# Performance work log

Measured on AMD Instinct MI355X. Metric: run time of the kernel, lower is better.

Reference implementation:

```python
import jax, jax.numpy as jnp
import numpy as np

N = 2048
E = 32768
IN_CH = 512
HID = 64
HEADS = 4
OUT_CH = 64
NUM_HOPS = 2
BETA = 0.5
NEG_SLOPE = 0.2
LN_EPS = 1e-5


def setup_inputs() -> dict:
    key = jax.random.key(0)
    ks = jax.random.split(key, 12)
    x = jax.random.normal(ks[0], (N, IN_CH), jnp.float32)
    edge_index = jax.random.randint(ks[1], (2, E), 0, N, dtype=jnp.int32)
    g = lambda k, shape, fan_in: jax.random.normal(k, shape, jnp.float32) * (1.0 / np.sqrt(fan_in))
    return {
        'x': x,
        'edge_index': edge_index,
        'l1_lin_w': g(ks[2], (NUM_HOPS, IN_CH, HEADS * HID), IN_CH),
        'l1_att_src': g(ks[3], (NUM_HOPS, HEADS, HID), HID),
        'l1_att_dst': g(ks[4], (NUM_HOPS, HEADS, HID), HID),
        'l1_hop_att': jnp.ones((NUM_HOPS,), jnp.float32),
        'l1_bias': g(ks[5], (HEADS * HID,), HEADS * HID),
        'l2_lin_w': g(ks[6], (NUM_HOPS, HEADS * HID, OUT_CH), HEADS * HID),
        'l2_att_src': g(ks[7], (NUM_HOPS, 1, OUT_CH), OUT_CH),
        'l2_att_dst': g(ks[8], (NUM_HOPS, 1, OUT_CH), OUT_CH),
        'l2_hop_att': jnp.ones((NUM_HOPS,), jnp.float32),
        'l2_res_w': g(ks[9], (HEADS * HID, OUT_CH), HEADS * HID),
        'l2_ln_scale': jnp.ones((OUT_CH,), jnp.float32),
        'l2_ln_bias': jnp.zeros((OUT_CH,), jnp.float32),
        'l2_bias': g(ks[10], (OUT_CH,), OUT_CH),
    }


def _leaky(v):
    return jnp.where(v >= 0, v, NEG_SLOPE * v)


def _masked_softmax_src(score, mask):
    # PyG softmax(alpha, edge_index[1]): normalize over src (axis 0) per dst column.
    s = jnp.where(mask[:, :, None], score, -jnp.inf)
    s = s - jnp.max(s, axis=0, keepdims=True)  # diag always valid -> finite max
    e = jnp.exp(s)
    return e / jnp.sum(e, axis=0, keepdims=True)


def _mgat_conv(x, A, motif, lin_w, att_src, att_dst, hop_att, heads, out_ch, concat,
               res_w=None, ln_scale=None, ln_bias=None, bias=None, residual=False):
    n = x.shape[0]
    hop_w = jax.nn.softmax(hop_att)
    eye = jnp.eye(n, dtype=bool)
    out = 0.0
    A_pow = A  # adj^(hop+1)
    for hop in range(NUM_HOPS):
        mask = (A_pow > 0) | eye  # remove_self_loops + add_self_loops -> diag always in
        hop_x = (x @ lin_w[hop]).reshape(n, heads, out_ch)
        s_src = jnp.einsum('nhc,hc->nh', hop_x, att_src[hop])
        s_dst = jnp.einsum('nhc,hc->nh', hop_x, att_dst[hop])
        score = s_src[:, None, :] + s_dst[None, :, :]  # [src, dst, h]
        a_first = _masked_softmax_src(_leaky(score), mask)
        a_motif = _masked_softmax_src(_leaky(score * motif[:, :, None]), mask)
        alpha = BETA * a_first + (1.0 - BETA) * a_motif
        hop_out = jnp.einsum('sdh,shc->dhc', alpha, hop_x)  # scatter-add at dst
        out = out + hop_w[hop] * hop_out
        A_pow = A_pow @ A
    if concat:
        out = out.reshape(n, heads * out_ch)
    else:
        out = out.mean(axis=1)
    if residual:
        res = x @ res_w if res_w is not None else x
        out = out + res
        mu = jnp.mean(out, axis=-1, keepdims=True)
        var = jnp.mean((out - mu) ** 2, axis=-1, keepdims=True)
        out = (out - mu) / jnp.sqrt(var + LN_EPS) * ln_scale + ln_bias
    if bias is not None:
        out = out + bias
    return out


def reference(x, edge_index, l1_lin_w, l1_att_src, l1_att_dst, l1_hop_att, l1_bias,
              l2_lin_w, l2_att_src, l2_att_dst, l2_hop_att, l2_res_w,
              l2_ln_scale, l2_ln_bias, l2_bias):
    n = x.shape[0]
    A = jnp.zeros((n, n), x.dtype).at[edge_index[0], edge_index[1]].set(1.0)
    motif = A @ A @ A
    motif = motif / jnp.maximum(motif.sum(axis=-1, keepdims=True), 1.0)
    h = _mgat_conv(x, A, motif, l1_lin_w, l1_att_src, l1_att_dst, l1_hop_att,
                   heads=HEADS, out_ch=HID, concat=True, bias=l1_bias, residual=False)
    h = jax.nn.elu(h)  # dropout p in eval mode -> identity
    out = _mgat_conv(h, A, motif, l2_lin_w, l2_att_src, l2_att_dst, l2_hop_att,
                     heads=1, out_ch=OUT_CH, concat=False,
                     res_w=l2_res_w, ln_scale=l2_ln_scale, ln_bias=l2_ln_bias,
                     bias=l2_bias, residual=True)
    return out
```

## Files before the change

kernel.cpp:

```cpp
#include <hip/hip_runtime.h>

namespace {

constexpr int kN = 2048;
constexpr int kWords = kN / 64;
constexpr int kC1 = 256;
constexpr int kC2 = 64;
constexpr int kIN = 512;
constexpr float kNegSlope = 0.2f;
constexpr float kLnEps = 1e-5f;

__device__ __forceinline__ float leakyf(float v) {
  return v >= 0.f ? v : kNegSlope * v;
}
__device__ __forceinline__ void onl(float& m, float& l, float v) {
  if (v > m) { l = l * __expf(m - v) + 1.f; m = v; }
  else       { l += __expf(v - m); }
}
__device__ __forceinline__ void mergeml(float& M, float& L, float m, float l) {
  if (m > M) { L = L * __expf(M - m) + l; M = m; }
  else       { L += l * __expf(m - M); }
}
__device__ __forceinline__ float bf2f(unsigned short u) {
  union { unsigned int i; float f; } v; v.i = ((unsigned int)u) << 16; return v.f;
}
__device__ __forceinline__ unsigned short f2bf(float f) {
  unsigned int u = __float_as_uint(f);
  unsigned int r = u + 0x7fffu + ((u >> 16) & 1u);
  return (unsigned short)(r >> 16);
}

__global__ void build_bits(const int* __restrict__ ei, int E,
                           unsigned long long* rowbits, unsigned long long* colbitsT) {
  int e = blockIdx.x * 256 + threadIdx.x;
  if (e >= E) return;
  int s = ei[e], d = ei[E + e];
  atomicOr(&rowbits[(size_t)s * kWords + (d >> 6)], 1ull << (d & 63));
  atomicOr(&colbitsT[(size_t)(s >> 6) * kN + d], 1ull << (s & 63));
}

__global__ __launch_bounds__(256) void a2_tiled(
    const unsigned long long* __restrict__ rowbits,
    const unsigned long long* __restrict__ colbitsT,
    unsigned short* __restrict__ A2,
    unsigned long long* __restrict__ colbits2T) {
  int bx = blockIdx.x, by = blockIdx.y;
  int t = threadIdx.x;
  __shared__ unsigned long long rb[64][33];
  __shared__ unsigned long long cb[32][64];
  __shared__ unsigned long long cw[64];
  int s0 = by * 64, d0 = bx * 64;
  for (int i = t; i < 64 * 32; i += 256) {
    int ss = i >> 5, w = i & 31;
    rb[ss][w] = rowbits[(size_t)(s0 + ss) * kWords + w];
  }
  for (int i = t; i < 32 * 64; i += 256) {
    int w = i >> 6, dd = i & 63;
    cb[w][dd] = colbitsT[(size_t)w * kN + d0 + dd];
  }
  if (t < 64) cw[t] = 0ull;
  __syncthreads();
  int tx = t & 15, ty4 = (t >> 4) * 4;
  int acc[4][4] = {};
#pragma unroll 4
  for (int w = 0; w < 32; ++w) {
    unsigned long long r0 = rb[ty4 + 0][w], r1 = rb[ty4 + 1][w];
    unsigned long long r2 = rb[ty4 + 2][w], r3 = rb[ty4 + 3][w];
    unsigned long long c0 = cb[w][tx], c1 = cb[w][tx + 16];
    unsigned long long c2 = cb[w][tx + 32], c3 = cb[w][tx + 48];
    acc[0][0] += __popcll(r0 & c0); acc[0][1] += __popcll(r0 & c1);
    acc[0][2] += __popcll(r0 & c2); acc[0][3] += __popcll(r0 & c3);
    acc[1][0] += __popcll(r1 & c0); acc[1][1] += __popcll(r1 & c1);
    acc[1][2] += __popcll(r1 & c2); acc[1][3] += __popcll(r1 & c3);
    acc[2][0] += __popcll(r2 & c0); acc[2][1] += __popcll(r2 & c1);
    acc[2][2] += __popcll(r2 & c2); acc[2][3] += __popcll(r2 & c3);
    acc[3][0] += __popcll(r3 & c0); acc[3][1] += __popcll(r3 & c1);
    acc[3][2] += __popcll(r3 & c2); acc[3][3] += __popcll(r3 & c3);
  }
#pragma unroll
  for (int i = 0; i < 4; ++i)
#pragma unroll
    for (int j = 0; j < 4; ++j)
      A2[(size_t)(s0 + ty4 + i) * kN + d0 + tx + 16 * j] = (unsigned short)acc[i][j];
#pragma unroll
  for (int j = 0; j < 4; ++j) {
    unsigned long long m = 0;
#pragma unroll
    for (int i = 0; i < 4; ++i)
      if (acc[i][j]) m |= 1ull << (ty4 + i);
    if (m) atomicOr(&cw[tx + 16 * j], m);
  }
  __syncthreads();
  if (t < 64) colbits2T[(size_t)by * kN + d0 + t] = cw[t];
}

__global__ __launch_bounds__(256) void a3_dense(
    const unsigned long long* __restrict__ rowbits,
    const unsigned short* __restrict__ A2,
    unsigned short* __restrict__ a3u,
    float* __restrict__ invr) {
  int s = blockIdx.x;
  int t = threadIdx.x;
  int lane = t & 63;
  __shared__ unsigned short jl[kN];
  __shared__ int jtot_s;
  __shared__ float redv[4];
  if (t < 64) {
    unsigned long long word = (lane < kWords) ? rowbits[(size_t)s * kWords + lane] : 0ull;
    int c = __popcll(word);
    int inc = c;
    for (int o = 1; o < 64; o <<= 1) { int v = __shfl_up(inc, o); if (lane >= o) inc += v; }
    if (lane == 63) jtot_s = inc;
    int off = inc - c;
    int base = lane * 64;
    while (word) {
      int b = __builtin_ctzll(word);
      word &= word - 1;
      jl[off++] = (unsigned short)(base + b);
    }
  }
  __syncthreads();
  int jtot = jtot_s;
  const uint4* a2v = reinterpret_cast<const uint4*>(A2);
  uint4 acc = make_uint4(0u, 0u, 0u, 0u);
  int ji = 0;
  for (; ji + 4 <= jtot; ji += 4) {
    uint4 v0 = a2v[(size_t)jl[ji + 0] * 256 + t];
    uint4 v1 = a2v[(size_t)jl[ji + 1] * 256 + t];
    uint4 v2 = a2v[(size_t)jl[ji + 2] * 256 + t];
    uint4 v3 = a2v[(size_t)jl[ji + 3] * 256 + t];
    acc.x += v0.x + v1.x + v2.x + v3.x;
    acc.y += v0.y + v1.y + v2.y + v3.y;
    acc.z += v0.z + v1.z + v2.z + v3.z;
    acc.w += v0.w + v1.w + v2.w + v3.w;
  }
  for (; ji < jtot; ++ji) {
    uint4 v = a2v[(size_t)jl[ji] * 256 + t];
    acc.x += v.x; acc.y += v.y; acc.z += v.z; acc.w += v.w;
  }
  reinterpret_cast<uint4*>(a3u)[(size_t)s * 256 + t] = acc;
  float tot = (float)((acc.x & 0xffffu) + (acc.x >> 16) +
                      (acc.y & 0xffffu) + (acc.y >> 16) +
                      (acc.z & 0xffffu) + (acc.z >> 16) +
                      (acc.w & 0xffffu) + (acc.w >> 16));
  for (int o = 32; o; o >>= 1) tot += __shfl_xor(tot, o);
  if (lane == 0) redv[t >> 6] = tot;
  __syncthreads();
  if (t == 0)
    invr[s] = 1.f / fmaxf(redv[0] + redv[1] + redv[2] + redv[3], 1.f);
}

__global__ __launch_bounds__(256) void transpose_motif(
    const unsigned short* __restrict__ a3u, const float* __restrict__ invr,
    float* __restrict__ motifT) {
  __shared__ float tile[64][65];
  __shared__ float invs[64];
  int d0 = blockIdx.x * 64, s0 = blockIdx.y * 64;
  int t = threadIdx.x;
  int tx = t & 63, ty = t >> 6;
  if (t < 64) invs[t] = invr[s0 + t];
  __syncthreads();
#pragma unroll
  for (int i = 0; i < 64; i += 4)
    tile[ty + i][tx] = (float)a3u[(size_t)(s0 + ty + i) * kN + d0 + tx] * invs[ty + i];
  __syncthreads();
#pragma unroll
  for (int i = 0; i < 64; i += 4)
    motifT[(size_t)(d0 + ty + i) * kN + s0 + tx] = tile[tx][ty + i];
}

__global__ __launch_bounds__(256) void gemm1(
    const float* __restrict__ x, const float* __restrict__ l1w,
    unsigned short* __restrict__ hx1b,
    const float* __restrict__ l1as, const float* __restrict__ l1ad,
    float* __restrict__ ss1, float* __restrict__ sd1) {
  int hop = blockIdx.z;
  int row0 = blockIdx.y * 32, col0 = blockIdx.x * 64;
  const float* B = l1w + (size_t)hop * kIN * kC1;
  unsigned short* Cz = hx1b + (size_t)hop * kN * kC1;
  __shared__ float As[2][32][20];
  __shared__ float Bs[2][16][68];
  int t = threadIdx.x;
  int tx = t & 15, ty = t >> 4;
  int am = t >> 2, ak = (t & 3) * 4;
  int bk = t >> 4, bn = (t & 15) * 4;
  float4 ra, rb;
  if (t < 128)
    ra = *reinterpret_cast<const float4*>(x + (size_t)(row0 + am) * kIN + ak);
  rb = *reinterpret_cast<const float4*>(B + (size_t)bk * kC1 + col0 + bn);
  if (t < 128)
    *reinterpret_cast<float4*>(&As[0][am][ak]) = ra;
  *reinterpret_cast<float4*>(&Bs[0][bk][bn]) = rb;
  __syncthreads();
  float acc[2][4] = {};
  int cur = 0;
  for (int k0 = 16; k0 <= kIN; k0 += 16) {
    bool more = (k0 < kIN);
    if (more) {
      if (t < 128)
        ra = *reinterpret_cast<const float4*>(x + (size_t)(row0 + am) * kIN + k0 + ak);
      rb = *reinterpret_cast<const float4*>(B + (size_t)(k0 + bk) * kC1 + col0 + bn);
    }
#pragma unroll
    for (int kk = 0; kk < 16; ++kk) {
      float a0 = As[cur][ty * 2 + 0][kk];
      float a1 = As[cur][ty * 2 + 1][kk];
      float4 b = *reinterpret_cast<const float4*>(&Bs[cur][kk][tx * 4]);
      acc[0][0] += a0 * b.x; acc[0][1] += a0 * b.y;
      acc[0][2] += a0 * b.z; acc[0][3] += a0 * b.w;
      acc[1][0] += a1 * b.x; acc[1][1] += a1 * b.y;
      acc[1][2] += a1 * b.z; acc[1][3] += a1 * b.w;
    }
    if (more) {
      if (t < 128)
        *reinterpret_cast<float4*>(&As[cur ^ 1][am][ak]) = ra;
      *reinterpret_cast<float4*>(&Bs[cur ^ 1][bk][bn]) = rb;
      __syncthreads();
      cur ^= 1;
    }
  }
#pragma unroll
  for (int i = 0; i < 2; ++i) {
    ushort4 pb;
    pb.x = f2bf(acc[i][0]); pb.y = f2bf(acc[i][1]);
    pb.z = f2bf(acc[i][2]); pb.w = f2bf(acc[i][3]);
    *reinterpret_cast<ushort4*>(Cz + (size_t)(row0 + ty * 2 + i) * kC1 + col0 + tx * 4) = pb;
  }
  int h = col0 >> 6;
  float as_[4], ad_[4];
#pragma unroll
  for (int j = 0; j < 4; ++j) {
    as_[j] = l1as[hop * kC1 + col0 + tx * 4 + j];
    ad_[j] = l1ad[hop * kC1 + col0 + tx * 4 + j];
  }
#pragma unroll
  for (int i = 0; i < 2; ++i) {
    float ps = acc[i][0] * as_[0] + acc[i][1] * as_[1] +
               acc[i][2] * as_[2] + acc[i][3] * as_[3];
    float pd = acc[i][0] * ad_[0] + acc[i][1] * ad_[1] +
               acc[i][2] * ad_[2] + acc[i][3] * ad_[3];
#pragma unroll
    for (int o = 1; o < 16; o <<= 1) {
      ps += __shfl_xor(ps, o);
      pd += __shfl_xor(pd, o);
    }
    if (tx == 0) {
      int n = row0 + ty * 2 + i;
      ss1[((size_t)hop * kN + n) * 4 + h] = ps;
      sd1[((size_t)hop * kN + n) * 4 + h] = pd;
    }
  }
}

__global__ __launch_bounds__(256) void gemm2(
    const float* __restrict__ A, const float* __restrict__ l2w,
    const float* __restrict__ l2rw, unsigned short* __restrict__ hx2b,
    float* __restrict__ resOut,
    const float* __restrict__ attS, const float* __restrict__ attD,
    float* __restrict__ ssO, float* __restrict__ sdO) {
  int z = blockIdx.z;
  const float* B = (z < 2) ? l2w + (size_t)z * kC1 * kC2 : l2rw;
  __shared__ float As[2][16][20];
  __shared__ float Bs[2][16][68];
  int t = threadIdx.x;
  int tx = t & 15, ty = t >> 4;
  int row0 = blockIdx.y * 16;
  int am = t >> 2, ak = (t & 3) * 4;
  int bk = t >> 4, bn = (t & 15) * 4;
  float4 ra, rb;
  if (t < 64)
    ra = *reinterpret_cast<const float4*>(A + (size_t)(row0 + am) * kC1 + ak);
  rb = *reinterpret_cast<const float4*>(B + (size_t)bk * kC2 + bn);
  if (t < 64)
    *reinterpret_cast<float4*>(&As[0][am][ak]) = ra;
  *reinterpret_cast<float4*>(&Bs[0][bk][bn]) = rb;
  __syncthreads();
  float acc[4] = {};
  int cur = 0;
  for (int k0 = 16; k0 <= kC1; k0 += 16) {
    bool more = (k0 < kC1);
    if (more) {
      if (t < 64)
        ra = *reinterpret_cast<const float4*>(A + (size_t)(row0 + am) * kC1 + k0 + ak);
      rb = *reinterpret_cast<const float4*>(B + (size_t)(k0 + bk) * kC2 + bn);
    }
#pragma unroll
    for (int kk = 0; kk < 16; ++kk) {
      float a = As[cur][ty][kk];
      float4 b = *reinterpret_cast<const float4*>(&Bs[cur][kk][tx * 4]);
      acc[0] += a * b.x; acc[1] += a * b.y;
      acc[2] += a * b.z; acc[3] += a * b.w;
    }
    if (more) {
      if (t < 64)
        *reinterpret_cast<float4*>(&As[cur ^ 1][am][ak]) = ra;
      *reinterpret_cast<float4*>(&Bs[cur ^ 1][bk][bn]) = rb;
      __syncthreads();
      cur ^= 1;
    }
  }
  if (z < 2) {
    ushort4 pb;
    pb.x = f2bf(acc[0]); pb.y = f2bf(acc[1]);
    pb.z = f2bf(acc[2]); pb.w = f2bf(acc[3]);
    *reinterpret_cast<ushort4*>(hx2b + (size_t)z * kN * kC2 +
                                (size_t)(row0 + ty) * kC2 + tx * 4) = pb;
    float as_[4], ad_[4];
#pragma unroll
    for (int j = 0; j < 4; ++j) {
      as_[j] = attS[z * kC2 + tx * 4 + j];
      ad_[j] = attD[z * kC2 + tx * 4 + j];
    }
    float ps = acc[0] * as_[0] + acc[1] * as_[1] + acc[2] * as_[2] + acc[3] * as_[3];
    float pd = acc[0] * ad_[0] + acc[1] * ad_[1] + acc[2] * ad_[2] + acc[3] * ad_[3];
#pragma unroll
    for (int o = 1; o < 16; o <<= 1) {
      ps += __shfl_xor(ps, o);
      pd += __shfl_xor(pd, o);
    }
    if (tx == 0) {
      int n = row0 + ty;
      ssO[(size_t)z * kN + n] = ps;
      sdO[(size_t)z * kN + n] = pd;
    }
  } else {
    float4 c = make_float4(acc[0], acc[1], acc[2], acc[3]);
    *reinterpret_cast<float4*>(resOut + (size_t)(row0 + ty) * kC2 + tx * 4) = c;
  }
}

__global__ __launch_bounds__(256) void agg_l1(
    const unsigned short* __restrict__ hxb,
    const float* __restrict__ ssrc,
    const float* __restrict__ sdst,
    const float* __restrict__ motifT,
    const unsigned long long* __restrict__ colbitsT,
    const unsigned long long* __restrict__ colbits2T,
    const float* __restrict__ hop_att,
    const float* __restrict__ bias,
    float* __restrict__ hbuf) {
  int d = blockIdx.x;
  int t = threadIdx.x;
  int lane = t & 63;
  int h = t >> 6;
  int cq = lane;
  int hq = cq >> 4;
  __shared__ unsigned short slist[kN];
  __shared__ float mrow[kN];
  __shared__ float w_lds[64 * 4];
  __shared__ int s_total;
  __shared__ float4 red4[4][64];
  {
    const float4* mp = reinterpret_cast<const float4*>(motifT + (size_t)d * kN);
    float4* mr = reinterpret_cast<float4*>(mrow);
    mr[t] = mp[t];
    mr[t + 256] = mp[t + 256];
  }
  float a0 = hop_att[0], a1 = hop_att[1];
  float mxa = fmaxf(a0, a1);
  float e0 = __expf(a0 - mxa), e1 = __expf(a1 - mxa);
  float wh0 = e0 / (e0 + e1), wh1 = e1 / (e0 + e1);
  float4 acc4 = make_float4(0.f, 0.f, 0.f, 0.f);
  for (int hop = 0; hop < 2; ++hop) {
    const unsigned long long* cm = hop ? colbits2T : colbitsT;
    if (t < 64) {
      unsigned long long word = (lane < kWords) ? cm[(size_t)lane * kN + d] : 0ull;
      if (lane == (d >> 6)) word |= 1ull << (d & 63);
      int cnt = __popcll(word);
      int inc = cnt;
      for (int o = 1; o < 64; o <<= 1) { int v = __shfl_up(inc, o); if (lane >= o) inc += v; }
      if (lane == 63) s_total = inc;
      int off = inc - cnt;
      int base = lane * 64;
      while (word) {
        int b = __builtin_ctzll(word);
        word &= word - 1;
        slist[off++] = (unsigned short)(base + b);
      }
    }
    __syncthreads();
    int total = s_total;
    float sd = sdst[((size_t)hop * kN + d) * 4 + h];
    const ushort4* hx4 = reinterpret_cast<const ushort4*>(hxb + (size_t)hop * kN * kC1);
    const float* ssp = ssrc + (size_t)hop * kN * 4;
    float m1 = -3.0e38f, l1v = 0.f, m2 = -3.0e38f, l2v = 0.f;
    for (int q = lane; q < total; q += 64) {
      int s = slist[q];
      float mv = mrow[s];
      float v = ssp[s * 4 + h] + sd;
      onl(m1, l1v, leakyf(v));
      onl(m2, l2v, leakyf(v * mv));
    }
#pragma unroll
    for (int o = 1; o < 64; o <<= 1) {
      float mm = __shfl_xor(m1, o), ll = __shfl_xor(l1v, o);
      mergeml(m1, l1v, mm, ll);
      float mm2 = __shfl_xor(m2, o), ll2 = __shfl_xor(l2v, o);
      mergeml(m2, l2v, mm2, ll2);
    }
    float il1 = 1.f / l1v, il2 = 1.f / l2v;
    float wh = hop ? wh1 : wh0;
    for (int c0 = 0; c0 < total; c0 += 64) {
      int nsi = min(64, total - c0);
      if (lane < nsi) {
        int s = slist[c0 + lane];
        float mv = mrow[s];
        float v = ssp[s * 4 + h] + sd;
        w_lds[lane * 4 + h] = (0.5f * __expf(leakyf(v) - m1) * il1 +
                               0.5f * __expf(leakyf(v * mv) - m2) * il2) * wh;
      }
      __syncthreads();
      int q = h;
      for (; q + 4 < nsi; q += 8) {
        int s0 = slist[c0 + q], s1 = slist[c0 + q + 4];
        ushort4 u0 = hx4[(size_t)s0 * 64 + cq];
        ushort4 u1 = hx4[(size_t)s1 * 64 + cq];
        float w0 = w_lds[q * 4 + hq], w1 = w_lds[(q + 4) * 4 + hq];
        acc4.x += w0 * bf2f(u0.x) + w1 * bf2f(u1.x);
        acc4.y += w0 * bf2f(u0.y) + w1 * bf2f(u1.y);
        acc4.z += w0 * bf2f(u0.z) + w1 * bf2f(u1.z);
        acc4.w += w0 * bf2f(u0.w) + w1 * bf2f(u1.w);
      }
      if (q < nsi) {
        int s0 = slist[c0 + q];
        ushort4 u0 = hx4[(size_t)s0 * 64 + cq];
        float w0 = w_lds[q * 4 + hq];
        acc4.x += w0 * bf2f(u0.x); acc4.y += w0 * bf2f(u0.y);
        acc4.z += w0 * bf2f(u0.z); acc4.w += w0 * bf2f(u0.w);
      }
      __syncthreads();
    }
    __syncthreads();
  }
  red4[h][cq] = acc4;
  __syncthreads();
  if (t < 64) {
    float4 a = red4[0][t], b = red4[1][t], c = red4[2][t], e = red4[3][t];
    float4 bv = reinterpret_cast<const float4*>(bias)[t];
    float4 v;
    v.x = a.x + b.x + c.x + e.x + bv.x;
    v.y = a.y + b.y + c.y + e.y + bv.y;
    v.z = a.z + b.z + c.z + e.z + bv.z;
    v.w = a.w + b.w + c.w + e.w + bv.w;
    v.x = v.x > 0.f ? v.x : __expf(v.x) - 1.f;
    v.y = v.y > 0.f ? v.y : __expf(v.y) - 1.f;
    v.z = v.z > 0.f ? v.z : __expf(v.z) - 1.f;
    v.w = v.w > 0.f ? v.w : __expf(v.w) - 1.f;
    reinterpret_cast<float4*>(hbuf)[(size_t)d * 64 + t] = v;
  }
}

__global__ __launch_bounds__(256) void agg_l2(
    const unsigned short* __restrict__ hxb,
    const float* __restrict__ ssrc,
    const float* __restrict__ sdst,
    const float* __restrict__ motifT,
    const unsigned long long* __restrict__ colbitsT,
    const unsigned long long* __restrict__ colbits2T,
    const float* __restrict__ hop_att,
    const float* __restrict__ res,
    const float* __restrict__ lns, const float* __restrict__ lnb,
    const float* __restrict__ l2b,
    float* __restrict__ out) {
  int d = blockIdx.x;
  int t = threadIdx.x;
  int lane = t & 63;
  int g = t >> 6;
  int cq = t & 15;
  int sg = t >> 4;
  __shared__ unsigned short slist[kN];
  __shared__ float mrow[kN];
  __shared__ float w_lds[64];
  __shared__ int s_total;
  __shared__ float4 red4[16][16];
  __shared__ float out_lds[64];
  __shared__ float smst[4][4];
  {
    const float4* mp = reinterpret_cast<const float4*>(motifT + (size_t)d * kN);
    float4* mr = reinterpret_cast<float4*>(mrow);
    mr[t] = mp[t];
    mr[t + 256] = mp[t + 256];
  }
  float a0 = hop_att[0], a1 = hop_att[1];
  float mxa = fmaxf(a0, a1);
  float e0 = __expf(a0 - mxa), e1 = __expf(a1 - mxa);
  float wh0 = e0 / (e0 + e1), wh1 = e1 / (e0 + e1);
  float4 acc4 = make_float4(0.f, 0.f, 0.f, 0.f);
  for (int hop = 0; hop < 2; ++hop) {
    const unsigned long long* cm = hop ? colbits2T : colbitsT;
    if (t < 64) {
      unsigned long long word = (lane < kWords) ? cm[(size_t)lane * kN + d] : 0ull;
      if (lane == (d >> 6)) word |= 1ull << (d & 63);
      int cnt = __popcll(word);
      int inc = cnt;
      for (int o = 1; o < 64; o <<= 1) { int v = __shfl_up(inc, o); if (lane >= o) inc += v; }
      if (lane == 63) s_total = inc;
      int off = inc - cnt;
      int base = lane * 64;
      while (word) {
        int b = __builtin_ctzll(word);
        word &= word - 1;
        slist[off++] = (unsigned short)(base + b);
      }
    }
    __syncthreads();
    int total = s_total;
    float sd = sdst[(size_t)hop * kN + d];
    const ushort4* hx4 = reinterpret_cast<const ushort4*>(hxb + (size_t)hop * kN * kC2);
    const float* ssp = ssrc + (size_t)hop * kN;
    float m1 = -3.0e38f, l1v = 0.f, m2 = -3.0e38f, l2v = 0.f;
    for (int q = t; q < total; q += 256) {
      int s = slist[q];
      float mv = mrow[s];
      float v = ssp[s] + sd;
      onl(m1, l1v, leakyf(v));
      onl(m2, l2v, leakyf(v * mv));
    }
#pragma unroll
    for (int o = 1; o < 64; o <<= 1) {
      float mm = __shfl_xor(m1, o), ll = __shfl_xor(l1v, o);
      mergeml(m1, l1v, mm, ll);
      float mm2 = __shfl_xor(m2, o), ll2 = __shfl_xor(l2v, o);
      mergeml(m2, l2v, mm2, ll2);
    }
    if (lane == 0) {
      smst[g][0] = m1; smst[g][1] = l1v; smst[g][2] = m2; smst[g][3] = l2v;
    }
    __syncthreads();
    float M1 = -3.0e38f, L1 = 0.f, M2 = -3.0e38f, L2 = 0.f;
#pragma unroll
    for (int gg = 0; gg < 4; ++gg) {
      mergeml(M1, L1, smst[gg][0], smst[gg][1]);
      mergeml(M2, L2, smst[gg][2], smst[gg][3]);
    }
    float il1 = 1.f / L1, il2 = 1.f / L2;
    float wh = hop ? wh1 : wh0;
    for (int c0 = 0; c0 < total; c0 += 64) {
      int nsi = min(64, total - c0);
      if (t < nsi) {
        int s = slist[c0 + t];
        float mv = mrow[s];
        float v = ssp[s] + sd;
        w_lds[t] = (0.5f * __expf(leakyf(v) - M1) * il1 +
                    0.5f * __expf(leakyf(v * mv) - M2) * il2) * wh;
      }
      __syncthreads();
      int q = sg;
      for (; q + 16 < nsi; q += 32) {
        int s0 = slist[c0 + q], s1 = slist[c0 + q + 16];
        ushort4 u0 = hx4[(size_t)s0 * 16 + cq];
        ushort4 u1 = hx4[(size_t)s1 * 16 + cq];
        float w0 = w_lds[q], w1 = w_lds[q + 16];
        acc4.x += w0 * bf2f(u0.x) + w1 * bf2f(u1.x);
        acc4.y += w0 * bf2f(u0.y) + w1 * bf2f(u1.y);
        acc4.z += w0 * bf2f(u0.z) + w1 * bf2f(u1.z);
        acc4.w += w0 * bf2f(u0.w) + w1 * bf2f(u1.w);
      }
      if (q < nsi) {
        int s0 = slist[c0 + q];
        ushort4 u0 = hx4[(size_t)s0 * 16 + cq];
        float w0 = w_lds[q];
        acc4.x += w0 * bf2f(u0.x); acc4.y += w0 * bf2f(u0.y);
        acc4.z += w0 * bf2f(u0.z); acc4.w += w0 * bf2f(u0.w);
      }
      __syncthreads();
    }
    __syncthreads();
  }
  red4[sg][cq] = acc4;
  __syncthreads();
  if (t < 16) {
    float4 v = make_float4(0.f, 0.f, 0.f, 0.f);
#pragma unroll
    for (int q = 0; q < 16; ++q) {
      float4 a = red4[q][t];
      v.x += a.x; v.y += a.y; v.z += a.z; v.w += a.w;
    }
    out_lds[t * 4 + 0] = v.x;
    out_lds[t * 4 + 1] = v.y;
    out_lds[t * 4 + 2] = v.z;
    out_lds[t * 4 + 3] = v.w;
  }
  __syncthreads();
  if (t < 64) {
    float v = out_lds[t] + res[(size_t)d * kC2 + t];
    float s = v;
    for (int o = 32; o; o >>= 1) s += __shfl_xor(s, o);
    float mu = s * (1.f / kC2);
    float dv = v - mu;
    float q = dv * dv;
    for (int o = 32; o; o >>= 1) q += __shfl_xor(q, o);
    float var = q * (1.f / kC2);
    out[(size_t)d * kC2 + t] = dv * rsqrtf(var + kLnEps) * lns[t] + lnb[t] + l2b[t];
  }
}

}

extern "C" void kernel_launch(void* const* d_in, const int* in_sizes, int n_in,
                              void* d_out, int out_size, void* d_ws, size_t ws_size,
                              hipStream_t stream) {
  const float* x    = (const float*)d_in[0];
  const int*   ei   = (const int*)d_in[1];
  const float* l1w  = (const float*)d_in[2];
  const float* l1as = (const float*)d_in[3];
  const float* l1ad = (const float*)d_in[4];
  const float* l1ha = (const float*)d_in[5];
  const float* l1b  = (const float*)d_in[6];
  const float* l2w  = (const float*)d_in[7];
  const float* l2as = (const float*)d_in[8];
  const float* l2ad = (const float*)d_in[9];
  const float* l2ha = (const float*)d_in[10];
  const float* l2rw = (const float*)d_in[11];
  const float* lns  = (const float*)d_in[12];
  const float* lnb  = (const float*)d_in[13];
  const float* l2b  = (const float*)d_in[14];
  int E = in_sizes[1] / 2;

  size_t o = 0;
  auto take = [&](size_t bytes) { size_t r = o; o += (bytes + 255) & ~(size_t)255; return r; };
  size_t oRB  = take((size_t)kN * kWords * 8);
  size_t oCB  = take((size_t)kWords * kN * 8);
  size_t zEnd = o;
  size_t oCB2 = take((size_t)kWords * kN * 8);
  size_t oA2  = take((size_t)kN * kN * 2);
  size_t oA3  = take((size_t)kN * kN * 2);
  size_t oINV = take((size_t)kN * 4);
  size_t oMFT = take((size_t)kN * kN * 4);
  size_t oHX1 = take((size_t)2 * kN * kC1 * 2);
  size_t oH   = take((size_t)kN * kC1 * 4);
  size_t oHX2 = take((size_t)2 * kN * kC2 * 2);
  size_t oRES = take((size_t)kN * kC2 * 4);
  size_t oSS1 = take((size_t)2 * kN * 4 * 4);
  size_t oSD1 = take((size_t)2 * kN * 4 * 4);
  size_t oSS2 = take((size_t)2 * kN * 4);
  size_t oSD2 = take((size_t)2 * kN * 4);
  if (ws_size < o) return;

  char* w = (char*)d_ws;
  unsigned long long* rowbits = (unsigned long long*)(w + oRB);
  unsigned long long* colbitsT = (unsigned long long*)(w + oCB);
  unsigned long long* colbits2T = (unsigned long long*)(w + oCB2);
  unsigned short* A2 = (unsigned short*)(w + oA2);
  unsigned short* A3u = (unsigned short*)(w + oA3);
  float* invr = (float*)(w + oINV);
  float* motifT = (float*)(w + oMFT);
  unsigned short* hx1b = (unsigned short*)(w + oHX1);
  float* hbuf = (float*)(w + oH);
  unsigned short* hx2b = (unsigned short*)(w + oHX2);
  float* res = (float*)(w + oRES);
  float* ss1 = (float*)(w + oSS1);
  float* sd1 = (float*)(w + oSD1);
  float* ss2 = (float*)(w + oSS2);
  float* sd2 = (float*)(w + oSD2);

  hipMemsetAsync(d_ws, 0, zEnd, stream);

  build_bits<<<(E + 255) / 256, 256, 0, stream>>>(ei, E, rowbits, colbitsT);
  a2_tiled<<<dim3(kN / 64, kN / 64), 256, 0, stream>>>(rowbits, colbitsT, A2, colbits2T);
  a3_dense<<<kN, 256, 0, stream>>>(rowbits, A2, A3u, invr);
  transpose_motif<<<dim3(kN / 64, kN / 64), 256, 0, stream>>>(A3u, invr, motifT);

  gemm1<<<dim3(kC1 / 64, kN / 32, 2), 256, 0, stream>>>(x, l1w, hx1b, l1as, l1ad, ss1, sd1);
  agg_l1<<<kN, 256, 0, stream>>>(hx1b, ss1, sd1, motifT, colbitsT, colbits2T,
                                 l1ha, l1b, hbuf);

  gemm2<<<dim3(1, kN / 16, 3), 256, 0, stream>>>(hbuf, l2w, l2rw, hx2b, res,
                                                 l2as, l2ad, ss2, sd2);
  agg_l2<<<kN, 256, 0, stream>>>(hx2b, ss2, sd2, motifT, colbitsT, colbits2T,
                                 l2ha, res, lns, lnb, l2b, (float*)d_out);
}
```

Before: 148.6 us.

## Double-buffer attention weights to drop a barrier per aggregation chunk

Both aggregation kernels now compute the softmax weights for the next 64-source chunk into a second LDS buffer while the current chunk is gathered, so each chunk needs one barrier instead of two. The first chunk's weights are computed in a prologue per hop. The extra end-of-hop barrier is removed and the l2 inner loop is restructured to match. This costs slightly more LDS and some register pressure from overlapping the weight computation with the gather.

```diff
diff --git a/kernel.cpp b/kernel.cpp
--- a/kernel.cpp
+++ b/kernel.cpp
@@ -347,7 +347,7 @@
   int hq = cq >> 4;
   __shared__ unsigned short slist[kN];
   __shared__ float mrow[kN];
-  __shared__ float w_lds[64 * 4];
+  __shared__ float w_lds[2][64 * 4];
   __shared__ int s_total;
   __shared__ float4 red4[4][64];
   {
@@ -400,22 +400,37 @@
     }
     float il1 = 1.f / l1v, il2 = 1.f / l2v;
     float wh = hop ? wh1 : wh0;
+    {
+      int nsi0 = min(64, total);
+      if (lane < nsi0) {
+        int s = slist[lane];
+        float mv = mrow[s];
+        float v = ssp[s * 4 + h] + sd;
+        w_lds[0][lane * 4 + h] = (0.5f * __expf(leakyf(v) - m1) * il1 +
+                                  0.5f * __expf(leakyf(v * mv) - m2) * il2) * wh;
+      }
+    }
+    __syncthreads();
+    int cur = 0;
     for (int c0 = 0; c0 < total; c0 += 64) {
       int nsi = min(64, total - c0);
-      if (lane < nsi) {
-        int s = slist[c0 + lane];
-        float mv = mrow[s];
-        float v = ssp[s * 4 + h] + sd;
-        w_lds[lane * 4 + h] = (0.5f * __expf(leakyf(v) - m1) * il1 +
-                               0.5f * __expf(leakyf(v * mv) - m2) * il2) * wh;
-      }
-      __syncthreads();
+      int c1 = c0 + 64;
+      if (c1 < total) {
+        int nsi1 = min(64, total - c1);
+        if (lane < nsi1) {
+          int s = slist[c1 + lane];
+          float mv = mrow[s];
+          float v = ssp[s * 4 + h] + sd;
+          w_lds[cur ^ 1][lane * 4 + h] = (0.5f * __expf(leakyf(v) - m1) * il1 +
+                                          0.5f * __expf(leakyf(v * mv) - m2) * il2) * wh;
+        }
+      }
       int q = h;
       for (; q + 4 < nsi; q += 8) {
         int s0 = slist[c0 + q], s1 = slist[c0 + q + 4];
         ushort4 u0 = hx4[(size_t)s0 * 64 + cq];
         ushort4 u1 = hx4[(size_t)s1 * 64 + cq];
-        float w0 = w_lds[q * 4 + hq], w1 = w_lds[(q + 4) * 4 + hq];
+        float w0 = w_lds[cur][q * 4 + hq], w1 = w_lds[cur][(q + 4) * 4 + hq];
         acc4.x += w0 * bf2f(u0.x) + w1 * bf2f(u1.x);
         acc4.y += w0 * bf2f(u0.y) + w1 * bf2f(u1.y);
         acc4.z += w0 * bf2f(u0.z) + w1 * bf2f(u1.z);
@@ -424,13 +439,13 @@
       if (q < nsi) {
         int s0 = slist[c0 + q];
         ushort4 u0 = hx4[(size_t)s0 * 64 + cq];
-        float w0 = w_lds[q * 4 + hq];
+        float w0 = w_lds[cur][q * 4 + hq];
         acc4.x += w0 * bf2f(u0.x); acc4.y += w0 * bf2f(u0.y);
         acc4.z += w0 * bf2f(u0.z); acc4.w += w0 * bf2f(u0.w);
       }
       __syncthreads();
-    }
-    __syncthreads();
+      cur ^= 1;
+    }
   }
   red4[h][cq] = acc4;
   __syncthreads();
@@ -470,7 +485,7 @@
   int sg = t >> 4;
   __shared__ unsigned short slist[kN];
   __shared__ float mrow[kN];
-  __shared__ float w_lds[64];
+  __shared__ float w_lds[2][64];
   __shared__ int s_total;
   __shared__ float4 red4[16][16];
   __shared__ float out_lds[64];
@@ -535,37 +550,53 @@
     }
     float il1 = 1.f / L1, il2 = 1.f / L2;
     float wh = hop ? wh1 : wh0;
+    {
+      int nsi0 = min(64, total);
+      if (t < nsi0) {
+        int s = slist[t];
+        float mv = mrow[s];
+        float v = ssp[s] + sd;
+        w_lds[0][t] = (0.5f * __expf(leakyf(v) - M1) * il1 +
+                       0.5f * __expf(leakyf(v * mv) - M2) * il2) * wh;
+      }
+    }
+    __syncthreads();
+    int cur = 0;
     for (int c0 = 0; c0 < total; c0 += 64) {
       int nsi = min(64, total - c0);
-      if (t < nsi) {
-        int s = slist[c0 + t];
-        float mv = mrow[s];
-        float v = ssp[s] + sd;
-        w_lds[t] = (0.5f * __expf(leakyf(v) - M1) * il1 +
-                    0.5f * __expf(leakyf(v * mv) - M2) * il2) * wh;
-      }
-      __syncthreads();
+      int c1 = c0 + 64;
+      if (c1 < total) {
+        int nsi1 = min(64, total - c1);
+        if (t < nsi1) {
+          int s = slist[c1 + t];
+          float mv = mrow[s];
+          float v = ssp[s] + sd;
+          w_lds[cur ^ 1][t] = (0.5f * __expf(leakyf(v) - M1) * il1 +
+                               0.5f * __expf(leakyf(v * mv) - M2) * il2) * wh;
+        }
+      }
       int q = sg;
-      for (; q + 16 < nsi; q += 32) {
+      if (q + 16 < nsi) {
         int s0 = slist[c0 + q], s1 = slist[c0 + q + 16];
         ushort4 u0 = hx4[(size_t)s0 * 16 + cq];
         ushort4 u1 = hx4[(size_t)s1 * 16 + cq];
-        float w0 = w_lds[q], w1 = w_lds[q + 16];
+        float w0 = w_lds[cur][q], w1 = w_lds[cur][q + 16];
         acc4.x += w0 * bf2f(u0.x) + w1 * bf2f(u1.x);
         acc4.y += w0 * bf2f(u0.y) + w1 * bf2f(u1.y);
         acc4.z += w0 * bf2f(u0.z) + w1 * bf2f(u1.z);
         acc4.w += w0 * bf2f(u0.w) + w1 * bf2f(u1.w);
-      }
-      if (q < nsi) {
+        q += 32;
+      }
+      for (; q < nsi; q += 16) {
         int s0 = slist[c0 + q];
         ushort4 u0 = hx4[(size_t)s0 * 16 + cq];
-        float w0 = w_lds[q];
+        float w0 = w_lds[cur][q];
         acc4.x += w0 * bf2f(u0.x); acc4.y += w0 * bf2f(u0.y);
         acc4.z += w0 * bf2f(u0.z); acc4.w += w0 * bf2f(u0.w);
       }
       __syncthreads();
-    }
-    __syncthreads();
+      cur ^= 1;
+    }
   }
   red4[sg][cq] = acc4;
   __syncthreads();
```

New measurement: 148.8 us. No clear change (+0.2%).

## Split aggregation kernels across two blocks per node with partial-sum combine

Applied to the files above, without the earlier changes.

Both attention aggregation kernels now launch two blocks per destination node. Each block handles half of the 64-source chunks and writes a partial sum. For layer 1, the bias+ELU epilogue moves into gemm2's A-load, which sums the two partials. For layer 2, a new combine kernel adds the partials and the residual, then applies LayerNorm. This doubles the grid to improve occupancy and load balance, at the cost of recomputing the softmax statistics and the motif-row load in both halves, extra partial-buffer traffic, and one more launch.

```diff
diff --git a/kernel.cpp b/kernel.cpp
--- a/kernel.cpp
+++ b/kernel.cpp
@@ -253,7 +253,9 @@
 }
 
 __global__ __launch_bounds__(256) void gemm2(
-    const float* __restrict__ A, const float* __restrict__ l2w,
+    const float* __restrict__ p1a, const float* __restrict__ p1b,
+    const float* __restrict__ l1b,
+    const float* __restrict__ l2w,
     const float* __restrict__ l2rw, unsigned short* __restrict__ hx2b,
     float* __restrict__ resOut,
     const float* __restrict__ attS, const float* __restrict__ attD,
@@ -267,9 +269,22 @@
   int row0 = blockIdx.y * 16;
   int am = t >> 2, ak = (t & 3) * 4;
   int bk = t >> 4, bn = (t & 15) * 4;
+  auto ldA = [&](int k) -> float4 {
+    size_t off = (size_t)(row0 + am) * kC1 + k + ak;
+    float4 a = *reinterpret_cast<const float4*>(p1a + off);
+    float4 b = *reinterpret_cast<const float4*>(p1b + off);
+    float4 c = *reinterpret_cast<const float4*>(l1b + k + ak);
+    float4 r;
+    r.x = a.x + b.x + c.x; r.y = a.y + b.y + c.y;
+    r.z = a.z + b.z + c.z; r.w = a.w + b.w + c.w;
+    r.x = r.x > 0.f ? r.x : __expf(r.x) - 1.f;
+    r.y = r.y > 0.f ? r.y : __expf(r.y) - 1.f;
+    r.z = r.z > 0.f ? r.z : __expf(r.z) - 1.f;
+    r.w = r.w > 0.f ? r.w : __expf(r.w) - 1.f;
+    return r;
+  };
   float4 ra, rb;
-  if (t < 64)
-    ra = *reinterpret_cast<const float4*>(A + (size_t)(row0 + am) * kC1 + ak);
+  if (t < 64) ra = ldA(0);
   rb = *reinterpret_cast<const float4*>(B + (size_t)bk * kC2 + bn);
   if (t < 64)
     *reinterpret_cast<float4*>(&As[0][am][ak]) = ra;
@@ -280,8 +295,7 @@
   for (int k0 = 16; k0 <= kC1; k0 += 16) {
     bool more = (k0 < kC1);
     if (more) {
-      if (t < 64)
-        ra = *reinterpret_cast<const float4*>(A + (size_t)(row0 + am) * kC1 + k0 + ak);
+      if (t < 64) ra = ldA(k0);
       rb = *reinterpret_cast<const float4*>(B + (size_t)(k0 + bk) * kC2 + bn);
     }
 #pragma unroll
@@ -337,9 +351,9 @@
     const unsigned long long* __restrict__ colbitsT,
     const unsigned long long* __restrict__ colbits2T,
     const float* __restrict__ hop_att,
-    const float* __restrict__ bias,
-    float* __restrict__ hbuf) {
+    float* __restrict__ part) {
   int d = blockIdx.x;
+  int half = blockIdx.y;
   int t = threadIdx.x;
   int lane = t & 63;
   int h = t >> 6;
@@ -400,7 +414,12 @@
     }
     float il1 = 1.f / l1v, il2 = 1.f / l2v;
     float wh = hop ? wh1 : wh0;
-    for (int c0 = 0; c0 < total; c0 += 64) {
+    int nch = (total + 63) >> 6;
+    int hc = (nch + 1) >> 1;
+    int cbeg = half * hc;
+    int cend = min(nch, cbeg + hc);
+    for (int ci = cbeg; ci < cend; ++ci) {
+      int c0 = ci * 64;
       int nsi = min(64, total - c0);
       if (lane < nsi) {
         int s = slist[c0 + lane];
@@ -436,17 +455,12 @@
   __syncthreads();
   if (t < 64) {
     float4 a = red4[0][t], b = red4[1][t], c = red4[2][t], e = red4[3][t];
-    float4 bv = reinterpret_cast<const float4*>(bias)[t];
     float4 v;
-    v.x = a.x + b.x + c.x + e.x + bv.x;
-    v.y = a.y + b.y + c.y + e.y + bv.y;
-    v.z = a.z + b.z + c.z + e.z + bv.z;
-    v.w = a.w + b.w + c.w + e.w + bv.w;
-    v.x = v.x > 0.f ? v.x : __expf(v.x) - 1.f;
-    v.y = v.y > 0.f ? v.y : __expf(v.y) - 1.f;
-    v.z = v.z > 0.f ? v.z : __expf(v.z) - 1.f;
-    v.w = v.w > 0.f ? v.w : __expf(v.w) - 1.f;
-    reinterpret_cast<float4*>(hbuf)[(size_t)d * 64 + t] = v;
+    v.x = a.x + b.x + c.x + e.x;
+    v.y = a.y + b.y + c.y + e.y;
+    v.z = a.z + b.z + c.z + e.z;
+    v.w = a.w + b.w + c.w + e.w;
+    reinterpret_cast<float4*>(part + ((size_t)half * kN + d) * kC1)[t] = v;
   }
 }
 
@@ -458,11 +472,9 @@
     const unsigned long long* __restrict__ colbitsT,
     const unsigned long long* __restrict__ colbits2T,
     const float* __restrict__ hop_att,
-    const float* __restrict__ res,
-    const float* __restrict__ lns, const float* __restrict__ lnb,
-    const float* __restrict__ l2b,
-    float* __restrict__ out) {
+    float* __restrict__ part) {
   int d = blockIdx.x;
+  int half = blockIdx.y;
   int t = threadIdx.x;
   int lane = t & 63;
   int g = t >> 6;
@@ -473,7 +485,6 @@
   __shared__ float w_lds[64];
   __shared__ int s_total;
   __shared__ float4 red4[16][16];
-  __shared__ float out_lds[64];
   __shared__ float smst[4][4];
   {
     const float4* mp = reinterpret_cast<const float4*>(motifT + (size_t)d * kN);
@@ -535,7 +546,12 @@
     }
     float il1 = 1.f / L1, il2 = 1.f / L2;
     float wh = hop ? wh1 : wh0;
-    for (int c0 = 0; c0 < total; c0 += 64) {
+    int nch = (total + 63) >> 6;
+    int hc = (nch + 1) >> 1;
+    int cbeg = half * hc;
+    int cend = min(nch, cbeg + hc);
+    for (int ci = cbeg; ci < cend; ++ci) {
+      int c0 = ci * 64;
       int nsi = min(64, total - c0);
       if (t < nsi) {
         int s = slist[c0 + t];
@@ -546,7 +562,7 @@
       }
       __syncthreads();
       int q = sg;
-      for (; q + 16 < nsi; q += 32) {
+      if (q + 16 < nsi) {
         int s0 = slist[c0 + q], s1 = slist[c0 + q + 16];
         ushort4 u0 = hx4[(size_t)s0 * 16 + cq];
         ushort4 u1 = hx4[(size_t)s1 * 16 + cq];
@@ -555,8 +571,9 @@
         acc4.y += w0 * bf2f(u0.y) + w1 * bf2f(u1.y);
         acc4.z += w0 * bf2f(u0.z) + w1 * bf2f(u1.z);
         acc4.w += w0 * bf2f(u0.w) + w1 * bf2f(u1.w);
-      }
-      if (q < nsi) {
+        q += 32;
+      }
+      for (; q < nsi; q += 16) {
         int s0 = slist[c0 + q];
         ushort4 u0 = hx4[(size_t)s0 * 16 + cq];
         float w0 = w_lds[q];
@@ -576,23 +593,28 @@
       float4 a = red4[q][t];
       v.x += a.x; v.y += a.y; v.z += a.z; v.w += a.w;
     }
-    out_lds[t * 4 + 0] = v.x;
-    out_lds[t * 4 + 1] = v.y;
-    out_lds[t * 4 + 2] = v.z;
-    out_lds[t * 4 + 3] = v.w;
-  }
-  __syncthreads();
-  if (t < 64) {
-    float v = out_lds[t] + res[(size_t)d * kC2 + t];
-    float s = v;
-    for (int o = 32; o; o >>= 1) s += __shfl_xor(s, o);
-    float mu = s * (1.f / kC2);
-    float dv = v - mu;
-    float q = dv * dv;
-    for (int o = 32; o; o >>= 1) q += __shfl_xor(q, o);
-    float var = q * (1.f / kC2);
-    out[(size_t)d * kC2 + t] = dv * rsqrtf(var + kLnEps) * lns[t] + lnb[t] + l2b[t];
-  }
+    reinterpret_cast<float4*>(part + ((size_t)half * kN + d) * kC2)[t] = v;
+  }
+}
+
+__global__ void combine_l2(
+    const float* __restrict__ part,
+    const float* __restrict__ res,
+    const float* __restrict__ lns, const float* __restrict__ lnb,
+    const float* __restrict__ l2b,
+    float* __restrict__ out) {
+  int d = blockIdx.x, t = threadIdx.x;
+  float v = part[((size_t)0 * kN + d) * kC2 + t] +
+            part[((size_t)1 * kN + d) * kC2 + t] +
+            res[(size_t)d * kC2 + t];
+  float s = v;
+  for (int o = 32; o; o >>= 1) s += __shfl_xor(s, o);
+  float mu = s * (1.f / kC2);
+  float dv = v - mu;
+  float q = dv * dv;
+  for (int o = 32; o; o >>= 1) q += __shfl_xor(q, o);
+  float var = q * (1.f / kC2);
+  out[(size_t)d * kC2 + t] = dv * rsqrtf(var + kLnEps) * lns[t] + lnb[t] + l2b[t];
 }
 
 }
@@ -628,8 +650,9 @@
   size_t oINV = take((size_t)kN * 4);
   size_t oMFT = take((size_t)kN * kN * 4);
   size_t oHX1 = take((size_t)2 * kN * kC1 * 2);
-  size_t oH   = take((size_t)kN * kC1 * 4);
+  size_t oP1  = take((size_t)2 * kN * kC1 * 4);
   size_t oHX2 = take((size_t)2 * kN * kC2 * 2);
+  size_t oP2  = take((size_t)2 * kN * kC2 * 4);
   size_t oRES = take((size_t)kN * kC2 * 4);
   size_t oSS1 = take((size_t)2 * kN * 4 * 4);
   size_t oSD1 = take((size_t)2 * kN * 4 * 4);
@@ -646,8 +669,9 @@
   float* invr = (float*)(w + oINV);
   float* motifT = (float*)(w + oMFT);
   unsigned short* hx1b = (unsigned short*)(w + oHX1);
-  float* hbuf = (float*)(w + oH);
+  float* p1 = (float*)(w + oP1);
   unsigned short* hx2b = (unsigned short*)(w + oHX2);
+  float* p2 = (float*)(w + oP2);
   float* res = (float*)(w + oRES);
   float* ss1 = (float*)(w + oSS1);
   float* sd1 = (float*)(w + oSD1);
@@ -662,11 +686,13 @@
   transpose_motif<<<dim3(kN / 64, kN / 64), 256, 0, stream>>>(A3u, invr, motifT);
 
   gemm1<<<dim3(kC1 / 64, kN / 32, 2), 256, 0, stream>>>(x, l1w, hx1b, l1as, l1ad, ss1, sd1);
-  agg_l1<<<kN, 256, 0, stream>>>(hx1b, ss1, sd1, motifT, colbitsT, colbits2T,
-                                 l1ha, l1b, hbuf);
-
-  gemm2<<<dim3(1, kN / 16, 3), 256, 0, stream>>>(hbuf, l2w, l2rw, hx2b, res,
+  agg_l1<<<dim3(kN, 2), 256, 0, stream>>>(hx1b, ss1, sd1, motifT, colbitsT, colbits2T,
+                                          l1ha, p1);
+
+  gemm2<<<dim3(1, kN / 16, 3), 256, 0, stream>>>(p1, p1 + (size_t)kN * kC1, l1b,
+                                                 l2w, l2rw, hx2b, res,
                                                  l2as, l2ad, ss2, sd2);
-  agg_l2<<<kN, 256, 0, stream>>>(hx2b, ss2, sd2, motifT, colbitsT, colbits2T,
-                                 l2ha, res, lns, lnb, l2b, (float*)d_out);
-}
+  agg_l2<<<dim3(kN, 2), 256, 0, stream>>>(hx2b, ss2, sd2, motifT, colbitsT, colbits2T,
+                                          l2ha, p2);
+  combine_l2<<<kN, 64, 0, stream>>>(p2, res, lns, lnb, l2b, (float*)d_out);
+}
```

Measured after the change: 169.7 us. +14.2%, slower.
